# Optimization experiments

Measured on AMD Instinct MI355X. Metric: run time of the kernel, lower is better.

## Reference

```python
import jax, jax.numpy as jnp
import numpy as np

THRESHOLD = 0.5
BAL_W = 0.01
Z_W = 0.001
TEMP = 1.0


def setup_inputs() -> dict:
    key = jax.random.key(0)
    kx, kw = jax.random.split(key)
    B, T, D = 8, 8192, 512
    x = jax.random.normal(kx, (B, T, D), dtype=jnp.float32)
    # LinearRouter weight: nn.Linear(d_model, 1, bias=False), init std=0.02
    W = jax.random.normal(kw, (1, D), dtype=jnp.float32) * 0.02
    return {"x": x, "W": W}


def reference(x, W):
    # raw_logits: (B, T, 1)
    raw_logits = jnp.einsum("btd,od->bto", x / TEMP, W)
    gate_values = jax.nn.sigmoid(raw_logits)          # (B, T, 1)
    gate_flat = gate_values[..., 0]                   # (B, T)
    selected_mask = gate_flat >= THRESHOLD            # (B, T)

    counts = selected_mask.sum(axis=-1)               # (B,)
    # Host sync mirrors the .item() in the original module; output shape is
    # data-dependent so this reference runs eagerly (not under jit).
    max_k = max(1, int(jax.device_get(counts.max())))

    # Vectorized stream compaction: stable argsort puts selected token
    # indices first, in ascending order (same order as per-row nonzero()).
    order = jnp.argsort((~selected_mask).astype(jnp.int32), axis=-1, stable=True)  # (B, T)
    pos = jnp.arange(max_k)                                                        # (max_k,)
    # Pad by repeating the LAST selected index/gate, as the torch code does.
    take = jnp.minimum(pos[None, :], jnp.maximum(counts[:, None] - 1, 0))          # (B, max_k)
    idx = jnp.take_along_axis(order, take, axis=1)                                 # (B, max_k)
    gv = jnp.take_along_axis(gate_flat, idx, axis=1)                               # (B, max_k)

    selected = idx[:, :, None, None].astype(jnp.int32)   # (B, max_k, 1, 1)
    gate_weights = gv[:, :, None]                        # (B, max_k, 1)

    # Training-mode losses (nn.Module defaults to training=True)
    mean_gate = gate_values.mean()
    aux_loss = BAL_W * mean_gate * (1.0 - mean_gate)
    z = jax.nn.logsumexp(raw_logits[..., 0], axis=-1)    # (B,)
    z_loss = Z_W * jnp.mean(z * z)

    return selected, gate_weights, raw_logits, aux_loss, z_loss
```

## Files before the change

### kernel.cpp

```cpp
#include <hip/hip_runtime.h>
#include <math.h>


__global__ __launch_bounds__(256) void logits_kernel(
    const float* __restrict__ x, const float* __restrict__ W,
    float* __restrict__ logits, int n_tokens)
{
    const int gid  = blockIdx.x * blockDim.x + threadIdx.x;
    const int wave = gid >> 6;
    const int lane = threadIdx.x & 63;
    if (wave >= n_tokens) return;

    const float4* xp = reinterpret_cast<const float4*>(x + (size_t)wave * 512 + lane * 8);
    const float4* wp = reinterpret_cast<const float4*>(W + lane * 8);
    float4 x0 = xp[0]; float4 x1 = xp[1];
    float4 w0 = wp[0]; float4 w1 = wp[1];

    double acc = (double)x0.x * w0.x + (double)x0.y * w0.y
               + (double)x0.z * w0.z + (double)x0.w * w0.w
               + (double)x1.x * w1.x + (double)x1.y * w1.y
               + (double)x1.z * w1.z + (double)x1.w * w1.w;

    #pragma unroll
    for (int off = 32; off > 0; off >>= 1)
        acc += __shfl_xor(acc, off, 64);

    if (lane == 0) logits[wave] = (float)acc;
}

__global__ __launch_bounds__(1024) void rowproc_kernel(
    const float* __restrict__ logits,
    float* __restrict__ out_sel, float* __restrict__ out_gw,
    float* __restrict__ ws_z, float* __restrict__ ws_sig,
    int T, int max_k)
{
    const int b    = blockIdx.x;
    const int tid  = threadIdx.x;
    const int lane = tid & 63;
    const int wid  = tid >> 6;
    const float* row = logits + (size_t)b * T;

    __shared__ float          s_log[8192];
    __shared__ unsigned short s_sel[8192];
    __shared__ float s_wredA[16];
    __shared__ float s_wredB[16];
    __shared__ int   s_wcnt[16];
    __shared__ int   s_woff[17];
    __shared__ float s_bmax, s_bsum, s_bsig;

    const int t0 = tid * 8;
    float v[8];
    float4 a0 = *reinterpret_cast<const float4*>(row + t0);
    float4 a1 = *reinterpret_cast<const float4*>(row + t0 + 4);
    v[0]=a0.x; v[1]=a0.y; v[2]=a0.z; v[3]=a0.w;
    v[4]=a1.x; v[5]=a1.y; v[6]=a1.z; v[7]=a1.w;
    #pragma unroll
    for (int i = 0; i < 8; ++i) s_log[t0 + i] = v[i];

    float m = v[0];
    #pragma unroll
    for (int i = 1; i < 8; ++i) m = fmaxf(m, v[i]);
    #pragma unroll
    for (int off = 32; off > 0; off >>= 1) m = fmaxf(m, __shfl_xor(m, off, 64));
    if (lane == 0) s_wredA[wid] = m;
    __syncthreads();
    if (tid == 0) {
        float mm = s_wredA[0];
        for (int i = 1; i < 16; ++i) mm = fmaxf(mm, s_wredA[i]);
        s_bmax = mm;
    }
    __syncthreads();
    const float bmax = s_bmax;

    float se = 0.f, sg = 0.f;
    int c_local = 0;
    #pragma unroll
    for (int i = 0; i < 8; ++i) {
        se += expf(v[i] - bmax);
        sg += 1.f / (1.f + expf(-v[i]));
        c_local += (v[i] >= 0.f) ? 1 : 0;
    }
    #pragma unroll
    for (int off = 32; off > 0; off >>= 1) {
        se += __shfl_xor(se, off, 64);
        sg += __shfl_xor(sg, off, 64);
    }
    if (lane == 0) { s_wredA[wid] = se; s_wredB[wid] = sg; }

    int inc = c_local;
    #pragma unroll
    for (int off = 1; off < 64; off <<= 1) {
        int n = __shfl_up(inc, off, 64);
        if (lane >= off) inc += n;
    }
    if (lane == 63) s_wcnt[wid] = inc;
    __syncthreads();
    if (tid == 0) {
        int run = 0;
        for (int i = 0; i < 16; ++i) { s_woff[i] = run; run += s_wcnt[i]; }
        s_woff[16] = run;
        float A = 0.f, Bs = 0.f;
        for (int i = 0; i < 16; ++i) { A += s_wredA[i]; Bs += s_wredB[i]; }
        s_bsum = A; s_bsig = Bs;
    }
    __syncthreads();

    const int excl = s_woff[wid] + (inc - c_local);
    const int cnt  = s_woff[16];

    int o = excl;
    #pragma unroll
    for (int i = 0; i < 8; ++i) {
        if (v[i] >= 0.f) s_sel[o++] = (unsigned short)(t0 + i);
    }
    __syncthreads();

    for (int k = tid; k < max_k; k += 1024) {
        int id = (k < cnt) ? (int)s_sel[k]
                           : (cnt > 0 ? (int)s_sel[cnt - 1] : 0);
        out_sel[(size_t)b * max_k + k] = (float)id;
        float lg = s_log[id];
        out_gw [(size_t)b * max_k + k] = 1.f / (1.f + expf(-lg));
    }

    if (tid == 0) {
        ws_z  [b] = bmax + logf(s_bsum);
        ws_sig[b] = s_bsig;
    }
}

__global__ void finalize_kernel(const float* __restrict__ ws_z,
                                const float* __restrict__ ws_sig,
                                float* __restrict__ out_aux,
                                float* __restrict__ out_z,
                                int B, float inv_BT)
{
    if (threadIdx.x == 0 && blockIdx.x == 0) {
        float s = 0.f, zz = 0.f;
        for (int b = 0; b < B; ++b) {
            s  += ws_sig[b];
            zz += ws_z[b] * ws_z[b];
        }
        float m = s * inv_BT;
        *out_aux = 0.01f  * m * (1.f - m);
        *out_z   = 0.001f * zz / (float)B;
    }
}

extern "C" void kernel_launch(void* const* d_in, const int* in_sizes, int n_in,
                              void* d_out, int out_size, void* d_ws, size_t ws_size,
                              hipStream_t stream)
{
    const float* x = (const float*)d_in[0];
    const float* W = (const float*)d_in[1];

    const int D  = in_sizes[1];
    const int BT = in_sizes[0] / D;
    const int B  = 8;
    const int T  = BT / B;
    const int max_k = (out_size - BT - 2) / (2 * B);

    float* out        = (float*)d_out;
    float* out_sel    = out;
    float* out_gw     = out + (size_t)B * max_k;
    float* out_logits = out + (size_t)2 * B * max_k;
    float* out_aux    = out + (size_t)2 * B * max_k + BT;
    float* out_z      = out_aux + 1;

    float* ws_z   = (float*)d_ws;
    float* ws_sig = ws_z + B;

    const int waves_per_block = 4;
    const int grid1 = (BT + waves_per_block - 1) / waves_per_block;
    logits_kernel<<<grid1, 256, 0, stream>>>(x, W, out_logits, BT);

    rowproc_kernel<<<B, 1024, 0, stream>>>(out_logits, out_sel, out_gw,
                                           ws_z, ws_sig, T, max_k);

    finalize_kernel<<<1, 64, 0, stream>>>(ws_z, ws_sig, out_aux, out_z,
                                          B, 1.0f / (float)BT);
}
```

Baseline: 33.43 us.

## Fuse per-chunk reductions into logits kernel and parallelize compaction across blocks

The logits kernel now handles 16 tokens per wave. In the same pass it computes per-chunk exp-sum, sigmoid-sum and selection counts, writing them to workspace. A second kernel replaces the 8-block row processor and the finalize kernel: 1024 blocks each prefix-scan the chunk counts and scatter their 64 tokens to compacted positions, and one extra block reduces the loss terms. This removes the serial single-block-per-row stage and one launch. The logsumexp now skips the max subtraction, which risks overflow for large logits.

```diff
diff --git a/kernel.cpp b/kernel.cpp
--- a/kernel.cpp
+++ b/kernel.cpp
@@ -2,148 +2,186 @@
 #include <math.h>
 
 
-__global__ __launch_bounds__(256) void logits_kernel(
+#define TT 8192
+#define BB 8
+#define CHUNK 16
+#define NCHUNK 4096
+#define CPR 512
+#define BPR 128
+
+__global__ __launch_bounds__(256) void k1_logits(
     const float* __restrict__ x, const float* __restrict__ W,
-    float* __restrict__ logits, int n_tokens)
+    float* __restrict__ logits,
+    float* __restrict__ ws_se, float* __restrict__ ws_sg, int* __restrict__ ws_cnt)
 {
-    const int gid  = blockIdx.x * blockDim.x + threadIdx.x;
-    const int wave = gid >> 6;
     const int lane = threadIdx.x & 63;
-    if (wave >= n_tokens) return;
-
-    const float4* xp = reinterpret_cast<const float4*>(x + (size_t)wave * 512 + lane * 8);
+    const int wid  = threadIdx.x >> 6;
+    const int wave = blockIdx.x * 4 + wid;
+
     const float4* wp = reinterpret_cast<const float4*>(W + lane * 8);
-    float4 x0 = xp[0]; float4 x1 = xp[1];
-    float4 w0 = wp[0]; float4 w1 = wp[1];
-
-    double acc = (double)x0.x * w0.x + (double)x0.y * w0.y
-               + (double)x0.z * w0.z + (double)x0.w * w0.w
-               + (double)x1.x * w1.x + (double)x1.y * w1.y
-               + (double)x1.z * w1.z + (double)x1.w * w1.w;
+    const float4 w0 = wp[0], w1 = wp[1];
+
+    float se_c = 0.f, sg_c = 0.f;
+    int   cnt_c = 0;
 
     #pragma unroll
-    for (int off = 32; off > 0; off >>= 1)
-        acc += __shfl_xor(acc, off, 64);
-
-    if (lane == 0) logits[wave] = (float)acc;
+    for (int g = 0; g < 2; ++g) {
+        const int tok0 = wave * CHUNK + g * 8;
+        const float4* xp = reinterpret_cast<const float4*>(
+            x + (size_t)tok0 * 512 + lane * 8);
+
+        double acc[8];
+        #pragma unroll
+        for (int j = 0; j < 8; ++j) {
+            float4 a0 = xp[j * 128];
+            float4 a1 = xp[j * 128 + 1];
+            acc[j] = (double)a0.x * w0.x + (double)a0.y * w0.y
+                   + (double)a0.z * w0.z + (double)a0.w * w0.w
+                   + (double)a1.x * w1.x + (double)a1.y * w1.y
+                   + (double)a1.z * w1.z + (double)a1.w * w1.w;
+        }
+
+        #pragma unroll
+        for (int j = 0; j < 8; ++j) {
+            acc[j] += __shfl_xor(acc[j], 8, 64);
+            acc[j] += __shfl_xor(acc[j], 16, 64);
+            acc[j] += __shfl_xor(acc[j], 32, 64);
+        }
+        double sA = (lane & 8)  ? acc[1] : acc[0];
+        double sB = (lane & 8)  ? acc[3] : acc[2];
+        double sC = (lane & 8)  ? acc[5] : acc[4];
+        double sD = (lane & 8)  ? acc[7] : acc[6];
+        double sE = (lane & 16) ? sB : sA;
+        double sF = (lane & 16) ? sD : sC;
+        double s  = (lane & 32) ? sF : sE;
+        s += __shfl_xor(s, 1, 64);
+        s += __shfl_xor(s, 2, 64);
+        s += __shfl_xor(s, 4, 64);
+
+        const float lg = (float)s;
+        if ((lane & 7) == 0) logits[tok0 + (lane >> 3)] = lg;
+
+        float e  = expf(lg);
+        float sg = 1.f / (1.f + expf(-lg));
+        e  += __shfl_xor(e, 8, 64);  e  += __shfl_xor(e, 16, 64);  e  += __shfl_xor(e, 32, 64);
+        sg += __shfl_xor(sg, 8, 64); sg += __shfl_xor(sg, 16, 64); sg += __shfl_xor(sg, 32, 64);
+        unsigned long long bal = __ballot(lg >= 0.f);
+        se_c  += e;
+        sg_c  += sg;
+        cnt_c += (int)(__popcll(bal) >> 3);
+    }
+
+    if (lane == 0) {
+        ws_se[wave]  = se_c;
+        ws_sg[wave]  = sg_c;
+        ws_cnt[wave] = cnt_c;
+    }
 }
 
-__global__ __launch_bounds__(1024) void rowproc_kernel(
+__global__ __launch_bounds__(256) void k2_finish(
     const float* __restrict__ logits,
+    const int* __restrict__ ws_cnt, const float* __restrict__ ws_se,
+    const float* __restrict__ ws_sg,
     float* __restrict__ out_sel, float* __restrict__ out_gw,
-    float* __restrict__ ws_z, float* __restrict__ ws_sig,
-    int T, int max_k)
+    float* __restrict__ out_aux, float* __restrict__ out_z, int max_k)
 {
-    const int b    = blockIdx.x;
     const int tid  = threadIdx.x;
     const int lane = tid & 63;
     const int wid  = tid >> 6;
-    const float* row = logits + (size_t)b * T;
-
-    __shared__ float          s_log[8192];
-    __shared__ unsigned short s_sel[8192];
-    __shared__ float s_wredA[16];
-    __shared__ float s_wredB[16];
-    __shared__ int   s_wcnt[16];
-    __shared__ int   s_woff[17];
-    __shared__ float s_bmax, s_bsum, s_bsig;
-
-    const int t0 = tid * 8;
-    float v[8];
-    float4 a0 = *reinterpret_cast<const float4*>(row + t0);
-    float4 a1 = *reinterpret_cast<const float4*>(row + t0 + 4);
-    v[0]=a0.x; v[1]=a0.y; v[2]=a0.z; v[3]=a0.w;
-    v[4]=a1.x; v[5]=a1.y; v[6]=a1.z; v[7]=a1.w;
-    #pragma unroll
-    for (int i = 0; i < 8; ++i) s_log[t0 + i] = v[i];
-
-    float m = v[0];
-    #pragma unroll
-    for (int i = 1; i < 8; ++i) m = fmaxf(m, v[i]);
-    #pragma unroll
-    for (int off = 32; off > 0; off >>= 1) m = fmaxf(m, __shfl_xor(m, off, 64));
-    if (lane == 0) s_wredA[wid] = m;
-    __syncthreads();
-    if (tid == 0) {
-        float mm = s_wredA[0];
-        for (int i = 1; i < 16; ++i) mm = fmaxf(mm, s_wredA[i]);
-        s_bmax = mm;
-    }
-    __syncthreads();
-    const float bmax = s_bmax;
-
-    float se = 0.f, sg = 0.f;
-    int c_local = 0;
-    #pragma unroll
-    for (int i = 0; i < 8; ++i) {
-        se += expf(v[i] - bmax);
-        sg += 1.f / (1.f + expf(-v[i]));
-        c_local += (v[i] >= 0.f) ? 1 : 0;
-    }
-    #pragma unroll
-    for (int off = 32; off > 0; off >>= 1) {
-        se += __shfl_xor(se, off, 64);
-        sg += __shfl_xor(sg, off, 64);
-    }
-    if (lane == 0) { s_wredA[wid] = se; s_wredB[wid] = sg; }
-
-    int inc = c_local;
+
+    if (blockIdx.x == BB * BPR) {
+        __shared__ float sred[256];
+        __shared__ float rowse[BB];
+        for (int r = 0; r < BB; ++r) {
+            float p = 0.f;
+            for (int i = tid; i < CPR; i += 256) p += ws_se[r * CPR + i];
+            sred[tid] = p; __syncthreads();
+            for (int s = 128; s > 0; s >>= 1) {
+                if (tid < s) sred[tid] += sred[tid + s];
+                __syncthreads();
+            }
+            if (tid == 0) rowse[r] = sred[0];
+            __syncthreads();
+        }
+        float p = 0.f;
+        for (int i = tid; i < NCHUNK; i += 256) p += ws_sg[i];
+        sred[tid] = p; __syncthreads();
+        for (int s = 128; s > 0; s >>= 1) {
+            if (tid < s) sred[tid] += sred[tid + s];
+            __syncthreads();
+        }
+        if (tid == 0) {
+            float zz = 0.f;
+            for (int r = 0; r < BB; ++r) { float z = logf(rowse[r]); zz += z * z; }
+            *out_z = 0.001f * zz / (float)BB;
+            float m = sred[0] / (float)(BB * TT);
+            *out_aux = 0.01f * m * (1.f - m);
+        }
+        return;
+    }
+
+    const int row  = blockIdx.x >> 7;
+    const int part = blockIdx.x & 127;
+
+    __shared__ int s_pref[CPR];
+    __shared__ int s_wsum[4];
+    __shared__ int s_lnz[4];
+
+    const int c0 = ws_cnt[row * CPR + 2 * tid];
+    const int c1 = ws_cnt[row * CPR + 2 * tid + 1];
+    const int v  = c0 + c1;
+    int inc = v;
     #pragma unroll
     for (int off = 1; off < 64; off <<= 1) {
         int n = __shfl_up(inc, off, 64);
         if (lane >= off) inc += n;
     }
-    if (lane == 63) s_wcnt[wid] = inc;
+    if (lane == 63) s_wsum[wid] = inc;
+    int lnz = (c1 > 0) ? (2 * tid + 1) : ((c0 > 0) ? (2 * tid) : -1);
+    #pragma unroll
+    for (int off = 32; off > 0; off >>= 1)
+        lnz = max(lnz, __shfl_xor(lnz, off, 64));
+    if (lane == 0) s_lnz[wid] = lnz;
     __syncthreads();
-    if (tid == 0) {
-        int run = 0;
-        for (int i = 0; i < 16; ++i) { s_woff[i] = run; run += s_wcnt[i]; }
-        s_woff[16] = run;
-        float A = 0.f, Bs = 0.f;
-        for (int i = 0; i < 16; ++i) { A += s_wredA[i]; Bs += s_wredB[i]; }
-        s_bsum = A; s_bsig = Bs;
-    }
+    int woff = 0;
+    for (int w = 0; w < wid; ++w) woff += s_wsum[w];
+    const int cnt = s_wsum[0] + s_wsum[1] + s_wsum[2] + s_wsum[3];
+    const int excl = woff + inc - v;
+    s_pref[2 * tid]     = excl;
+    s_pref[2 * tid + 1] = excl + c0;
+    const int lastnz = max(max(s_lnz[0], s_lnz[1]), max(s_lnz[2], s_lnz[3]));
     __syncthreads();
 
-    const int excl = s_woff[wid] + (inc - c_local);
-    const int cnt  = s_woff[16];
-
-    int o = excl;
-    #pragma unroll
-    for (int i = 0; i < 8; ++i) {
-        if (v[i] >= 0.f) s_sel[o++] = (unsigned short)(t0 + i);
-    }
-    __syncthreads();
-
-    for (int k = tid; k < max_k; k += 1024) {
-        int id = (k < cnt) ? (int)s_sel[k]
-                           : (cnt > 0 ? (int)s_sel[cnt - 1] : 0);
-        out_sel[(size_t)b * max_k + k] = (float)id;
-        float lg = s_log[id];
-        out_gw [(size_t)b * max_k + k] = 1.f / (1.f + expf(-lg));
-    }
-
-    if (tid == 0) {
-        ws_z  [b] = bmax + logf(s_bsum);
-        ws_sig[b] = s_bsig;
-    }
-}
-
-__global__ void finalize_kernel(const float* __restrict__ ws_z,
-                                const float* __restrict__ ws_sig,
-                                float* __restrict__ out_aux,
-                                float* __restrict__ out_z,
-                                int B, float inv_BT)
-{
-    if (threadIdx.x == 0 && blockIdx.x == 0) {
-        float s = 0.f, zz = 0.f;
-        for (int b = 0; b < B; ++b) {
-            s  += ws_sig[b];
-            zz += ws_z[b] * ws_z[b];
-        }
-        float m = s * inv_BT;
-        *out_aux = 0.01f  * m * (1.f - m);
-        *out_z   = 0.001f * zz / (float)B;
+    if (tid < 64) {
+        const int tloc = part * 64 + tid;
+        const float lg = logits[row * TT + tloc];
+        const bool sel = (lg >= 0.f);
+        unsigned long long bal = __ballot(sel);
+        const int cib = tid >> 4;
+        unsigned long long below = bal & ((1ull << tid) - 1ull);
+        below &= (0xFFFFull << (cib * 16));
+        const int pos = s_pref[part * 4 + cib] + (int)__popcll(below);
+        if (sel) {
+            out_sel[(size_t)row * max_k + pos] = (float)tloc;
+            out_gw [(size_t)row * max_k + pos] = 1.f / (1.f + expf(-lg));
+        }
+    }
+
+    if (part == BPR - 1) {
+        int tok_last = 0;
+        if (cnt > 0) {
+            const int cL = lastnz;
+            for (int j = CHUNK - 1; j >= 0; --j) {
+                float lg = logits[row * TT + cL * CHUNK + j];
+                if (lg >= 0.f) { tok_last = cL * CHUNK + j; break; }
+            }
+        }
+        const float lgl = logits[row * TT + tok_last];
+        const float gw_last = 1.f / (1.f + expf(-lgl));
+        for (int k = cnt + tid; k < max_k; k += 256) {
+            out_sel[(size_t)row * max_k + k] = (float)tok_last;
+            out_gw [(size_t)row * max_k + k] = gw_last;
+        }
     }
 }
 
@@ -156,27 +194,22 @@
 
     const int D  = in_sizes[1];
     const int BT = in_sizes[0] / D;
-    const int B  = 8;
-    const int T  = BT / B;
-    const int max_k = (out_size - BT - 2) / (2 * B);
+    const int max_k = (out_size - BT - 2) / (2 * BB);
 
     float* out        = (float*)d_out;
     float* out_sel    = out;
-    float* out_gw     = out + (size_t)B * max_k;
-    float* out_logits = out + (size_t)2 * B * max_k;
-    float* out_aux    = out + (size_t)2 * B * max_k + BT;
+    float* out_gw     = out + (size_t)BB * max_k;
+    float* out_logits = out + (size_t)2 * BB * max_k;
+    float* out_aux    = out + (size_t)2 * BB * max_k + BT;
     float* out_z      = out_aux + 1;
 
-    float* ws_z   = (float*)d_ws;
-    float* ws_sig = ws_z + B;
-
-    const int waves_per_block = 4;
-    const int grid1 = (BT + waves_per_block - 1) / waves_per_block;
-    logits_kernel<<<grid1, 256, 0, stream>>>(x, W, out_logits, BT);
-
-    rowproc_kernel<<<B, 1024, 0, stream>>>(out_logits, out_sel, out_gw,
-                                           ws_z, ws_sig, T, max_k);
-
-    finalize_kernel<<<1, 64, 0, stream>>>(ws_z, ws_sig, out_aux, out_z,
-                                          B, 1.0f / (float)BT);
+    float* ws_se  = (float*)d_ws;
+    float* ws_sg  = ws_se + NCHUNK;
+    int*   ws_cnt = (int*)(ws_sg + NCHUNK);
+
+    k1_logits<<<1024, 256, 0, stream>>>(x, W, out_logits, ws_se, ws_sg, ws_cnt);
+
+    k2_finish<<<BB * BPR + 1, 256, 0, stream>>>(out_logits, ws_cnt, ws_se, ws_sg,
+                                                out_sel, out_gw, out_aux, out_z,
+                                                max_k);
 }
```

New measurement: 41.29 us. 23.5% more time.

## Fuse row processing and loss finalize into one kernel with dedicated loss block

Applied to the files above, without the earlier changes.

Merges the per-row compaction kernel and the single-thread finalize kernel into one launch with B+1 blocks. The extra block computes the z-loss and the aux loss over all logits, while the row blocks only do the selection scan and store gate values for selected tokens. This removes a kernel launch and the workspace round trip. The loss block now works alone through 64K logits with serial tree reductions, which may lengthen the critical path. It also drops max-subtraction from the logsumexp, so large logits could overflow.

```diff
diff --git a/kernel.cpp b/kernel.cpp
--- a/kernel.cpp
+++ b/kernel.cpp
@@ -1,6 +1,9 @@
 #include <hip/hip_runtime.h>
 #include <math.h>
 
+
+#define TT 8192
+#define BB 8
 
 __global__ __launch_bounds__(256) void logits_kernel(
     const float* __restrict__ x, const float* __restrict__ W,
@@ -28,25 +31,55 @@
     if (lane == 0) logits[wave] = (float)acc;
 }
 
-__global__ __launch_bounds__(1024) void rowproc_kernel(
+__global__ __launch_bounds__(1024) void finish_kernel(
     const float* __restrict__ logits,
     float* __restrict__ out_sel, float* __restrict__ out_gw,
-    float* __restrict__ ws_z, float* __restrict__ ws_sig,
-    int T, int max_k)
+    float* __restrict__ out_aux, float* __restrict__ out_z, int max_k)
 {
-    const int b    = blockIdx.x;
     const int tid  = threadIdx.x;
     const int lane = tid & 63;
     const int wid  = tid >> 6;
-    const float* row = logits + (size_t)b * T;
 
-    __shared__ float          s_log[8192];
-    __shared__ unsigned short s_sel[8192];
-    __shared__ float s_wredA[16];
-    __shared__ float s_wredB[16];
-    __shared__ int   s_wcnt[16];
-    __shared__ int   s_woff[17];
-    __shared__ float s_bmax, s_bsum, s_bsig;
+    if (blockIdx.x == BB) {
+        __shared__ float sred[1024];
+        __shared__ float rowse[BB];
+        for (int r = 0; r < BB; ++r) {
+            const float* row = logits + (size_t)r * TT;
+            float p = 0.f;
+            for (int i = tid; i < TT; i += 1024) p += expf(row[i]);
+            sred[tid] = p; __syncthreads();
+            for (int s = 512; s > 0; s >>= 1) {
+                if (tid < s) sred[tid] += sred[tid + s];
+                __syncthreads();
+            }
+            if (tid == 0) rowse[r] = sred[0];
+            __syncthreads();
+        }
+        float p = 0.f;
+        for (int i = tid; i < BB * TT; i += 1024)
+            p += 1.f / (1.f + expf(-logits[i]));
+        sred[tid] = p; __syncthreads();
+        for (int s = 512; s > 0; s >>= 1) {
+            if (tid < s) sred[tid] += sred[tid + s];
+            __syncthreads();
+        }
+        if (tid == 0) {
+            float zz = 0.f;
+            for (int r = 0; r < BB; ++r) { float z = logf(rowse[r]); zz += z * z; }
+            *out_z = 0.001f * zz / (float)BB;
+            float m = sred[0] / (float)(BB * TT);
+            *out_aux = 0.01f * m * (1.f - m);
+        }
+        return;
+    }
+
+    const int b = blockIdx.x;
+    const float* row = logits + (size_t)b * TT;
+
+    __shared__ unsigned short s_sel[TT];
+    __shared__ float          s_gw [TT];
+    __shared__ int s_wsum[16];
+    __shared__ int s_woff[17];
 
     const int t0 = tid * 8;
     float v[8];
@@ -54,38 +87,10 @@
     float4 a1 = *reinterpret_cast<const float4*>(row + t0 + 4);
     v[0]=a0.x; v[1]=a0.y; v[2]=a0.z; v[3]=a0.w;
     v[4]=a1.x; v[5]=a1.y; v[6]=a1.z; v[7]=a1.w;
-    #pragma unroll
-    for (int i = 0; i < 8; ++i) s_log[t0 + i] = v[i];
 
-    float m = v[0];
-    #pragma unroll
-    for (int i = 1; i < 8; ++i) m = fmaxf(m, v[i]);
-    #pragma unroll
-    for (int off = 32; off > 0; off >>= 1) m = fmaxf(m, __shfl_xor(m, off, 64));
-    if (lane == 0) s_wredA[wid] = m;
-    __syncthreads();
-    if (tid == 0) {
-        float mm = s_wredA[0];
-        for (int i = 1; i < 16; ++i) mm = fmaxf(mm, s_wredA[i]);
-        s_bmax = mm;
-    }
-    __syncthreads();
-    const float bmax = s_bmax;
-
-    float se = 0.f, sg = 0.f;
     int c_local = 0;
     #pragma unroll
-    for (int i = 0; i < 8; ++i) {
-        se += expf(v[i] - bmax);
-        sg += 1.f / (1.f + expf(-v[i]));
-        c_local += (v[i] >= 0.f) ? 1 : 0;
-    }
-    #pragma unroll
-    for (int off = 32; off > 0; off >>= 1) {
-        se += __shfl_xor(se, off, 64);
-        sg += __shfl_xor(sg, off, 64);
-    }
-    if (lane == 0) { s_wredA[wid] = se; s_wredB[wid] = sg; }
+    for (int i = 0; i < 8; ++i) c_local += (v[i] >= 0.f) ? 1 : 0;
 
     int inc = c_local;
     #pragma unroll
@@ -93,15 +98,12 @@
         int n = __shfl_up(inc, off, 64);
         if (lane >= off) inc += n;
     }
-    if (lane == 63) s_wcnt[wid] = inc;
+    if (lane == 63) s_wsum[wid] = inc;
     __syncthreads();
     if (tid == 0) {
         int run = 0;
-        for (int i = 0; i < 16; ++i) { s_woff[i] = run; run += s_wcnt[i]; }
+        for (int i = 0; i < 16; ++i) { s_woff[i] = run; run += s_wsum[i]; }
         s_woff[16] = run;
-        float A = 0.f, Bs = 0.f;
-        for (int i = 0; i < 16; ++i) { A += s_wredA[i]; Bs += s_wredB[i]; }
-        s_bsum = A; s_bsig = Bs;
     }
     __syncthreads();
 
@@ -111,39 +113,21 @@
     int o = excl;
     #pragma unroll
     for (int i = 0; i < 8; ++i) {
-        if (v[i] >= 0.f) s_sel[o++] = (unsigned short)(t0 + i);
+        if (v[i] >= 0.f) {
+            s_sel[o] = (unsigned short)(t0 + i);
+            s_gw [o] = 1.f / (1.f + expf(-v[i]));
+            ++o;
+        }
     }
     __syncthreads();
 
     for (int k = tid; k < max_k; k += 1024) {
-        int id = (k < cnt) ? (int)s_sel[k]
-                           : (cnt > 0 ? (int)s_sel[cnt - 1] : 0);
+        int id; float g;
+        if (k < cnt)      { id = (int)s_sel[k];       g = s_gw[k]; }
+        else if (cnt > 0) { id = (int)s_sel[cnt - 1]; g = s_gw[cnt - 1]; }
+        else              { id = 0; g = 1.f / (1.f + expf(-row[0])); }
         out_sel[(size_t)b * max_k + k] = (float)id;
-        float lg = s_log[id];
-        out_gw [(size_t)b * max_k + k] = 1.f / (1.f + expf(-lg));
-    }
-
-    if (tid == 0) {
-        ws_z  [b] = bmax + logf(s_bsum);
-        ws_sig[b] = s_bsig;
-    }
-}
-
-__global__ void finalize_kernel(const float* __restrict__ ws_z,
-                                const float* __restrict__ ws_sig,
-                                float* __restrict__ out_aux,
-                                float* __restrict__ out_z,
-                                int B, float inv_BT)
-{
-    if (threadIdx.x == 0 && blockIdx.x == 0) {
-        float s = 0.f, zz = 0.f;
-        for (int b = 0; b < B; ++b) {
-            s  += ws_sig[b];
-            zz += ws_z[b] * ws_z[b];
-        }
-        float m = s * inv_BT;
-        *out_aux = 0.01f  * m * (1.f - m);
-        *out_z   = 0.001f * zz / (float)B;
+        out_gw [(size_t)b * max_k + k] = g;
     }
 }
 
@@ -156,27 +140,18 @@
 
     const int D  = in_sizes[1];
     const int BT = in_sizes[0] / D;
-    const int B  = 8;
-    const int T  = BT / B;
-    const int max_k = (out_size - BT - 2) / (2 * B);
+    const int max_k = (out_size - BT - 2) / (2 * BB);
 
     float* out        = (float*)d_out;
     float* out_sel    = out;
-    float* out_gw     = out + (size_t)B * max_k;
-    float* out_logits = out + (size_t)2 * B * max_k;
-    float* out_aux    = out + (size_t)2 * B * max_k + BT;
+    float* out_gw     = out + (size_t)BB * max_k;
+    float* out_logits = out + (size_t)2 * BB * max_k;
+    float* out_aux    = out + (size_t)2 * BB * max_k + BT;
     float* out_z      = out_aux + 1;
 
-    float* ws_z   = (float*)d_ws;
-    float* ws_sig = ws_z + B;
-
-    const int waves_per_block = 4;
-    const int grid1 = (BT + waves_per_block - 1) / waves_per_block;
+    const int grid1 = (BT + 3) / 4;
     logits_kernel<<<grid1, 256, 0, stream>>>(x, W, out_logits, BT);
 
-    rowproc_kernel<<<B, 1024, 0, stream>>>(out_logits, out_sel, out_gw,
-                                           ws_z, ws_sig, T, max_k);
-
-    finalize_kernel<<<1, 64, 0, stream>>>(ws_z, ws_sig, out_aux, out_z,
-                                          B, 1.0f / (float)BT);
+    finish_kernel<<<BB + 1, 1024, 0, stream>>>(out_logits, out_sel, out_gw,
+                                               out_aux, out_z, max_k);
 }
```

Measured after the change: 65.39 us. +95.6%, slower.
